# Performance work log

Hardware: AMD Instinct MI355X
Metric: run time of the kernel (lower is better)

The kernel has to match this reference:

```python
import jax, jax.numpy as jnp
import numpy as np

B, T, C, H, D = 128, 256, 384, 6, 64  # batch, seq (block_size), embed_dim, heads, head_size
FF = 4 * C


def _layernorm(x, g, b, eps=1e-5):
    mu = jnp.mean(x, axis=-1, keepdims=True)
    var = jnp.var(x, axis=-1, keepdims=True)
    return (x - mu) * jax.lax.rsqrt(var + eps) * g + b


def setup_inputs() -> dict:
    key = jax.random.key(0)
    ks = jax.random.split(key, 16)
    w = lambda k, shape: (jax.random.normal(k, shape, jnp.float32) * 0.02)
    return {
        "x": jax.random.normal(ks[0], (B, T, C), jnp.float32),
        "ln1_g": jnp.ones((C,), jnp.float32),
        "ln1_b": jnp.zeros((C,), jnp.float32),
        "Wk": w(ks[1], (H, C, D)), "bk": jnp.zeros((H, D), jnp.float32),
        "Wq": w(ks[2], (H, C, D)), "bq": jnp.zeros((H, D), jnp.float32),
        "Wv": w(ks[3], (H, C, D)), "bv": jnp.zeros((H, D), jnp.float32),
        "Wp": w(ks[4], (C, C)), "bp": jnp.zeros((C,), jnp.float32),
        "ln2_g": jnp.ones((C,), jnp.float32),
        "ln2_b": jnp.zeros((C,), jnp.float32),
        "W1": w(ks[5], (C, FF)), "b1": jnp.zeros((FF,), jnp.float32),
        "W2": w(ks[6], (FF, C)), "b2": jnp.zeros((C,), jnp.float32),
    }


def reference(x, ln1_g, ln1_b, Wk, bk, Wq, bq, Wv, bv, Wp, bp, ln2_g, ln2_b, W1, b1, W2, b2):
    # pre-LN attention branch
    h = _layernorm(x, ln1_g, ln1_b)
    # per-head projections, batched over heads: (B,T,C) x (H,C,D) -> (B,H,T,D)
    K = jnp.einsum("btc,hcd->bhtd", h, Wk) + bk[None, :, None, :]
    Q = jnp.einsum("btc,hcd->bhtd", h, Wq) + bq[None, :, None, :]
    V = jnp.einsum("btc,hcd->bhtd", h, Wv) + bv[None, :, None, :]
    # NOTE: original computes K @ Q^T scaled by embed_dim**-0.5 (faithful quirk)
    scores = jnp.einsum("bhtd,bhsd->bhts", K, Q) * (C ** -0.5)
    causal = jnp.tril(jnp.ones((T, T), dtype=bool))  # keep s <= t
    scores = jnp.where(causal[None, None], scores, -jnp.inf)
    attn = jax.nn.softmax(scores, axis=-1)  # dropout = identity (eval mode)
    out = jnp.einsum("bhts,bhsd->bhtd", attn, V)
    out = out.transpose(0, 2, 1, 3).reshape(B, T, C)  # concat heads
    x = x + out @ Wp + bp
    # pre-LN FFN branch
    h2 = _layernorm(x, ln2_g, ln2_b)
    x = x + jax.nn.relu(h2 @ W1 + b1) @ W2 + b2
    return x
```

## Files before the change

### kernel.cpp

```cpp
#include <hip/hip_runtime.h>
#include <stdint.h>

#define BB 128
#define TT 256
#define CC 384
#define HH 6
#define DD 64
#define FFF 1536
#define ROWS (BB*TT)

#define FCH 16384
#define NFC (ROWS/FCH)

typedef unsigned short u16;
typedef __bf16 bf8v __attribute__((ext_vector_type(8)));
typedef float f4v __attribute__((ext_vector_type(4)));

__device__ __forceinline__ float bf2f(u16 u) {
    unsigned int v = ((unsigned int)u) << 16;
    float f;
    __builtin_memcpy(&f, &v, 4);
    return f;
}
__device__ __forceinline__ u16 f2bf(float f) {
    unsigned int u;
    __builtin_memcpy(&u, &f, 4);
    u += 0x7fffu + ((u >> 16) & 1u);
    return (u16)(u >> 16);
}

__device__ __forceinline__ void gload_lds16(const void* g, void* l) {
    __builtin_amdgcn_global_load_lds(
        (__attribute__((address_space(1))) void*)(g),
        (__attribute__((address_space(3))) void*)(l), 16, 0, 0);
}

__device__ __forceinline__ void ln_body(
    int row, const float* __restrict__ x, const float* __restrict__ g,
    const float* __restrict__ b, u16* __restrict__ out, int lane)
{
    const float* xr = x + (long long)row * CC;
    float v[6]; float s = 0.f;
#pragma unroll
    for (int i = 0; i < 6; ++i) { v[i] = xr[lane + i * 64]; s += v[i]; }
#pragma unroll
    for (int o = 32; o > 0; o >>= 1) s += __shfl_xor(s, o);
    const float mu = s * (1.f / CC);
    float q = 0.f;
#pragma unroll
    for (int i = 0; i < 6; ++i) { float d = v[i] - mu; q += d * d; }
#pragma unroll
    for (int o = 32; o > 0; o >>= 1) q += __shfl_xor(q, o);
    const float inv = rsqrtf(q * (1.f / CC) + 1e-5f);
    u16* orow = out + (long long)row * CC;
#pragma unroll
    for (int i = 0; i < 6; ++i) {
        int c = lane + i * 64;
        orow[c] = f2bf((v[i] - mu) * inv * g[c] + b[c]);
    }
}

__global__ __launch_bounds__(256) void ln_kernel(
    const float* __restrict__ x, const float* __restrict__ g,
    const float* __restrict__ b, u16* __restrict__ out)
{
    ln_body(blockIdx.x * 4 + (threadIdx.x >> 6), x, g, b, out, threadIdx.x & 63);
}

__global__ __launch_bounds__(256) void ln1_cvt_kernel(
    const float* __restrict__ x, const float* __restrict__ ln1g, const float* __restrict__ ln1b,
    u16* __restrict__ h,
    const float* __restrict__ Wq, const float* __restrict__ Wk, const float* __restrict__ Wv,
    const float* __restrict__ bq, const float* __restrict__ bk, const float* __restrict__ bv,
    const float* __restrict__ Wp, const float* __restrict__ W1, const float* __restrict__ W2,
    u16* __restrict__ wqkvT, u16* __restrict__ wpT, u16* __restrict__ w1T,
    u16* __restrict__ w2T, float* __restrict__ bqkv)
{
    if (blockIdx.x < ROWS / 4) {
        ln_body(blockIdx.x * 4 + (threadIdx.x >> 6), x, ln1g, ln1b, h, threadIdx.x & 63);
        return;
    }
    const int S0 = 1152 * 384, S1 = 384 * 384, S2 = 1536 * 384, S3 = 384 * 1536;
    int i = (blockIdx.x - ROWS / 4) * 256 + threadIdx.x;
    if (i < S0) {
        int n = i / 384, k = i % 384;
        const float* W = (n < 384) ? Wq : (n < 768) ? Wk : Wv;
        int nn = (n >= 768) ? n - 768 : (n >= 384) ? n - 384 : n;
        int hh = nn >> 6, d = nn & 63;
        wqkvT[i] = f2bf(W[hh * (384 * 64) + k * 64 + d]);
        return;
    }
    i -= S0;
    if (i < S1) { int n = i / 384, k = i % 384; wpT[i] = f2bf(Wp[k * 384 + n]); return; }
    i -= S1;
    if (i < S2) { int n = i / 384, k = i % 384; w1T[i] = f2bf(W1[k * 1536 + n]); return; }
    i -= S2;
    if (i < S3) { int n = i / 1536, k = i % 1536; w2T[i] = f2bf(W2[k * 384 + n]); return; }
    i -= S3;
    if (i < 1152) bqkv[i] = (i < 384) ? bq[i] : (i < 768) ? bk[i - 384] : bv[i - 768];
}

__global__ __launch_bounds__(256) void vtrans_kernel(
    const u16* __restrict__ qkv, u16* __restrict__ vt)
{
    __shared__ u16 tile[64][65];
    const int z = blockIdx.x;
    const int tb = blockIdx.y;
    const int zb = z / HH, zh = z % HH;
    const u16* src = qkv + ((long long)(zb * TT + tb * 64)) * 1152 + 768 + zh * 64;
    const int tid = threadIdx.x;
#pragma unroll
    for (int it = 0; it < 16; ++it) {
        int idx = it * 256 + tid; int tl = idx >> 6, d = idx & 63;
        tile[tl][d] = src[(long long)tl * 1152 + d];
    }
    __syncthreads();
    u16* dst = vt + (long long)z * 64 * 256 + tb * 64;
#pragma unroll
    for (int it = 0; it < 16; ++it) {
        int idx = it * 256 + tid; int d = idx >> 6, tl = idx & 63;
        dst[(long long)d * 256 + tl] = tile[tl][d];
    }
}

__global__ __launch_bounds__(256) void flash_kernel(
    const u16* __restrict__ qkv, const u16* __restrict__ vt, u16* __restrict__ attnout)
{
    __shared__ __align__(16) u16 Pl[128 * 72];

    const int bh = blockIdx.x;
    const int half = blockIdx.y;
    const int b = bh / HH, hh = bh % HH;
    const int tid = threadIdx.x;
    const int wave = tid >> 6, lane = tid & 63;
    const int quad = lane >> 4, lq = lane & 15;
    const int t0 = half * 128;

    const long long qrow = (long long)b * TT * 1152;
    const u16* Kb  = qkv + qrow + 384 + hh * 64;
    const u16* Qb  = qkv + qrow + hh * 64;
    const u16* Vtb = vt + (long long)bh * (DD * TT);

    bf8v af[2][2];
#pragma unroll
    for (int i = 0; i < 2; ++i)
#pragma unroll
        for (int ks = 0; ks < 2; ++ks)
            af[i][ks] = *(const bf8v*)(Kb + (long long)(t0 + wave * 32 + i * 16 + lq) * 1152
                                          + ks * 32 + quad * 8);

    float m_run[2][4], l_run[2][4];
    f4v oacc[2][4];
#pragma unroll
    for (int i = 0; i < 2; ++i) {
#pragma unroll
        for (int r = 0; r < 4; ++r) { m_run[i][r] = -1e30f; l_run[i][r] = 0.f; }
#pragma unroll
        for (int j = 0; j < 4; ++j) oacc[i][j] = (f4v){0.f, 0.f, 0.f, 0.f};
    }

    const float scs = 0.05103103630798287f;
    const int ntiles = 2 * (half + 1);
    for (int st = 0; st < ntiles; ++st) {
        const int s0 = st * 64;
        f4v sacc[2][4];
#pragma unroll
        for (int i = 0; i < 2; ++i)
#pragma unroll
            for (int j = 0; j < 4; ++j) sacc[i][j] = (f4v){0.f, 0.f, 0.f, 0.f};
#pragma unroll
        for (int ks = 0; ks < 2; ++ks) {
            bf8v bq[4];
#pragma unroll
            for (int j = 0; j < 4; ++j)
                bq[j] = *(const bf8v*)(Qb + (long long)(s0 + j * 16 + lq) * 1152
                                          + ks * 32 + quad * 8);
#pragma unroll
            for (int i = 0; i < 2; ++i)
#pragma unroll
                for (int j = 0; j < 4; ++j)
                    sacc[i][j] = __builtin_amdgcn_mfma_f32_16x16x32_bf16(af[i][ks], bq[j], sacc[i][j], 0, 0, 0);
        }
#pragma unroll
        for (int i = 0; i < 2; ++i)
#pragma unroll
            for (int j = 0; j < 4; ++j)
#pragma unroll
                for (int r = 0; r < 4; ++r) {
                    int t_g = t0 + wave * 32 + i * 16 + quad * 4 + r;
                    int s_g = s0 + j * 16 + lq;
                    float v = sacc[i][j][r] * scs;
                    sacc[i][j][r] = (s_g <= t_g) ? v : -1e30f;
                }
#pragma unroll
        for (int i = 0; i < 2; ++i)
#pragma unroll
            for (int r = 0; r < 4; ++r) {
                float mt = sacc[i][0][r];
#pragma unroll
                for (int j = 1; j < 4; ++j) mt = fmaxf(mt, sacc[i][j][r]);
#pragma unroll
                for (int o = 8; o > 0; o >>= 1) mt = fmaxf(mt, __shfl_xor(mt, o));
                const float mn = fmaxf(m_run[i][r], mt);
                const float alpha = __expf(m_run[i][r] - mn);
                float rs = 0.f;
#pragma unroll
                for (int j = 0; j < 4; ++j) {
                    float e = __expf(sacc[i][j][r] - mn);
                    sacc[i][j][r] = e; rs += e;
                }
#pragma unroll
                for (int o = 8; o > 0; o >>= 1) rs += __shfl_xor(rs, o);
                m_run[i][r] = mn;
                l_run[i][r] = l_run[i][r] * alpha + rs;
#pragma unroll
                for (int j = 0; j < 4; ++j) oacc[i][j][r] *= alpha;
            }
#pragma unroll
        for (int i = 0; i < 2; ++i)
#pragma unroll
            for (int j = 0; j < 4; ++j)
#pragma unroll
                for (int r = 0; r < 4; ++r)
                    Pl[(wave * 32 + i * 16 + quad * 4 + r) * 72 + j * 16 + lq] = f2bf(sacc[i][j][r]);
#pragma unroll
        for (int ks2 = 0; ks2 < 2; ++ks2) {
            bf8v ap[2], bv_[4];
#pragma unroll
            for (int i = 0; i < 2; ++i)
                ap[i] = *(const bf8v*)(Pl + (wave * 32 + i * 16 + lq) * 72 + ks2 * 32 + quad * 8);
#pragma unroll
            for (int j = 0; j < 4; ++j)
                bv_[j] = *(const bf8v*)(Vtb + (long long)(j * 16 + lq) * 256 + s0 + ks2 * 32 + quad * 8);
#pragma unroll
            for (int i = 0; i < 2; ++i)
#pragma unroll
                for (int j = 0; j < 4; ++j)
                    oacc[i][j] = __builtin_amdgcn_mfma_f32_16x16x32_bf16(ap[i], bv_[j], oacc[i][j], 0, 0, 0);
        }
    }
#pragma unroll
    for (int i = 0; i < 2; ++i)
#pragma unroll
        for (int r = 0; r < 4; ++r) {
            const float inv = 1.f / l_run[i][r];
            u16* orow = attnout + ((long long)(b * TT + t0 + wave * 32 + i * 16 + quad * 4 + r)) * CC + hh * 64;
#pragma unroll
            for (int j = 0; j < 4; ++j)
                orow[j * 16 + lq] = f2bf(oacc[i][j][r] * inv);
        }
}

template<int BM, int BN, bool OUTBF, bool RELU, bool HASRES>
__global__ __launch_bounds__(256) void gemm_bt(
    const u16* __restrict__ A, const u16* __restrict__ Bw, void* __restrict__ Cp,
    const float* __restrict__ bias, const float* __restrict__ res,
    int K, int lda, int ldb, int ldc,
    long long sAb, long long sAh, long long sBb, long long sBh,
    long long sCb, long long sCh, int Hb, float scale)
{
    __shared__ __align__(16) u16 As[BM * 32];
    __shared__ __align__(16) u16 Bs[BN * 32];

    const int tid = threadIdx.x;
    const int wave = tid >> 6, lane = tid & 63;
    const int quad = lane >> 4, lq = lane & 15;

    const int z = blockIdx.z;
    const int zb = z / Hb, zh = z % Hb;
    const int m0 = blockIdx.x * BM;
    const int n0 = blockIdx.y * BN;

    A  += (long long)zb * sAb + (long long)zh * sAh + (long long)m0 * lda;
    Bw += (long long)zb * sBb + (long long)zh * sBh + (long long)n0 * ldb;
    const long long coff = (long long)zb * sCb + (long long)zh * sCh;

    constexpr int WM = BM / 2, WN = BN / 2;
    constexpr int MT = WM / 16, NT = WN / 16;
    const int wm0 = (wave >> 1) * WM;
    const int wn0 = (wave & 1) * WN;

    f4v acc[MT][NT];
#pragma unroll
    for (int i = 0; i < MT; ++i)
#pragma unroll
        for (int j = 0; j < NT; ++j) acc[i][j] = (f4v){0.f, 0.f, 0.f, 0.f};

    constexpr int AIT = BM / 64;
    constexpr int BIT = BN / 64;

    for (int k0 = 0; k0 < K; k0 += 32) {
        __syncthreads();
#pragma unroll
        for (int j = 0; j < AIT; ++j) {
            int idx = j * 256 + tid; int r = idx >> 2, pg = idx & 3;
            int lg = pg ^ ((r >> 1) & 3);
            gload_lds16(A + (long long)r * lda + k0 + lg * 8, As + idx * 8);
        }
#pragma unroll
        for (int j = 0; j < BIT; ++j) {
            int idx = j * 256 + tid; int r = idx >> 2, pg = idx & 3;
            int lg = pg ^ ((r >> 1) & 3);
            gload_lds16(Bw + (long long)r * ldb + k0 + lg * 8, Bs + idx * 8);
        }
        __syncthreads();

        bf8v af[MT], bfr[NT];
#pragma unroll
        for (int i = 0; i < MT; ++i) {
            int row = wm0 + i * 16 + lq;
            int pg = quad ^ ((row >> 1) & 3);
            af[i] = *(const bf8v*)(As + row * 32 + pg * 8);
        }
#pragma unroll
        for (int j = 0; j < NT; ++j) {
            int row = wn0 + j * 16 + lq;
            int pg = quad ^ ((row >> 1) & 3);
            bfr[j] = *(const bf8v*)(Bs + row * 32 + pg * 8);
        }
#pragma unroll
        for (int i = 0; i < MT; ++i)
#pragma unroll
            for (int j = 0; j < NT; ++j)
                acc[i][j] = __builtin_amdgcn_mfma_f32_16x16x32_bf16(af[i], bfr[j], acc[i][j], 0, 0, 0);
    }

#pragma unroll
    for (int i = 0; i < MT; ++i) {
#pragma unroll
        for (int j = 0; j < NT; ++j) {
            const int gcol = n0 + wn0 + j * 16 + lq;
            const float bcol = bias ? bias[gcol] : 0.f;
#pragma unroll
            for (int r = 0; r < 4; ++r) {
                const int grow = m0 + wm0 + i * 16 + quad * 4 + r;
                const long long off = coff + (long long)grow * ldc + gcol;
                float v = acc[i][j][r] * scale + bcol;
                if (HASRES) v += res[off];
                if (RELU)   v = fmaxf(v, 0.f);
                if (OUTBF)  ((u16*)Cp)[off] = f2bf(v);
                else        ((float*)Cp)[off] = v;
            }
        }
    }
}

extern "C" void kernel_launch(void* const* d_in, const int* in_sizes, int n_in,
                              void* d_out, int out_size, void* d_ws, size_t ws_size,
                              hipStream_t stream)
{
    const float* x    = (const float*)d_in[0];
    const float* ln1g = (const float*)d_in[1];
    const float* ln1b = (const float*)d_in[2];
    const float* Wk   = (const float*)d_in[3];
    const float* bk   = (const float*)d_in[4];
    const float* Wq   = (const float*)d_in[5];
    const float* bq   = (const float*)d_in[6];
    const float* Wv   = (const float*)d_in[7];
    const float* bv   = (const float*)d_in[8];
    const float* Wp   = (const float*)d_in[9];
    const float* bp   = (const float*)d_in[10];
    const float* ln2g = (const float*)d_in[11];
    const float* ln2b = (const float*)d_in[12];
    const float* W1   = (const float*)d_in[13];
    const float* b1   = (const float*)d_in[14];
    const float* W2   = (const float*)d_in[15];
    const float* b2   = (const float*)d_in[16];

    char* ws = (char*)d_ws;
    size_t off = 0;
    auto alloc = [&](size_t bytes) -> char* {
        char* p = ws + off; off += (bytes + 255) & ~(size_t)255; return p;
    };
    u16*   wqkvT = (u16*)alloc((size_t)1152 * 384 * 2);
    u16*   wpT   = (u16*)alloc((size_t)384 * 384 * 2);
    u16*   w1T   = (u16*)alloc((size_t)1536 * 384 * 2);
    u16*   w2T   = (u16*)alloc((size_t)384 * 1536 * 2);
    float* bqkv  = (float*)alloc((size_t)1152 * 4);
    u16*   h     = (u16*)alloc((size_t)ROWS * CC * 2);
    u16*   qkv   = (u16*)alloc((size_t)ROWS * 1152 * 2);
    u16*   vtff  = (u16*)alloc((size_t)FCH * FFF * 2);
    u16* attnout = h;
    u16* h2      = h;
    float* x1    = (float*)qkv;
    u16*   vt    = vtff;
    u16*   ff    = vtff;

    ln1_cvt_kernel<<<ROWS / 4 + 6918, 256, 0, stream>>>(
        x, ln1g, ln1b, h, Wq, Wk, Wv, bq, bk, bv, Wp, W1, W2,
        wqkvT, wpT, w1T, w2T, bqkv);
    gemm_bt<128, 128, true, false, false><<<dim3(ROWS / 128, 1152 / 128, 1), 256, 0, stream>>>(
        h, wqkvT, qkv, bqkv, nullptr, 384, 384, 384, 1152,
        0, 0, 0, 0, 0, 0, 1, 1.f);
    vtrans_kernel<<<dim3(BB * HH, 4), 256, 0, stream>>>(qkv, vt);
    flash_kernel<<<dim3(BB * HH, 2), 256, 0, stream>>>(qkv, vt, attnout);
    gemm_bt<128, 128, false, false, true><<<dim3(ROWS / 128, CC / 128, 1), 256, 0, stream>>>(
        attnout, wpT, x1, bp, x, CC, CC, CC, CC,
        0, 0, 0, 0, 0, 0, 1, 1.f);
    ln_kernel<<<ROWS / 4, 256, 0, stream>>>(x1, ln2g, ln2b, h2);
    for (int fc = 0; fc < NFC; ++fc) {
        const long long ro = (long long)fc * FCH;
        gemm_bt<128, 128, true, true, false><<<dim3(FCH / 128, FFF / 128, 1), 256, 0, stream>>>(
            h2 + ro * CC, w1T, ff, b1, nullptr, CC, CC, CC, FFF,
            0, 0, 0, 0, 0, 0, 1, 1.f);
        gemm_bt<128, 128, false, false, true><<<dim3(FCH / 128, CC / 128, 1), 256, 0, stream>>>(
            ff, w2T, (float*)d_out + ro * CC, b2, x1 + ro * CC, FFF, FFF, FFF, CC,
            0, 0, 0, 0, 0, 0, 1, 1.f);
    }
}
```

Before: 447.9 us.

## Split flash attention into 64-row query blocks and run FFN unchunked when workspace allows

The flash kernel now gives each block 64 query rows (16 per wave) instead of 128, launching four blocks per batch-head. The aim is better causal load balance and more, smaller blocks with fewer registers each. The FFN loop now runs as a single chunk when the workspace can hold the full intermediate, which removes one pair of GEMM launches and the partial-wave tails. The trade-off is less reuse of each K/V tile per block, so Q and V are loaded from global memory more times in total.

```diff
diff --git a/kernel.cpp b/kernel.cpp
--- a/kernel.cpp
+++ b/kernel.cpp
@@ -8,9 +8,6 @@
 #define DD 64
 #define FFF 1536
 #define ROWS (BB*TT)
-
-#define FCH 16384
-#define NFC (ROWS/FCH)
 
 typedef unsigned short u16;
 typedef __bf16 bf8v __attribute__((ext_vector_type(8)));
@@ -126,48 +123,41 @@
 __global__ __launch_bounds__(256) void flash_kernel(
     const u16* __restrict__ qkv, const u16* __restrict__ vt, u16* __restrict__ attnout)
 {
-    __shared__ __align__(16) u16 Pl[128 * 72];
-
-    const int bh = blockIdx.x;
-    const int half = blockIdx.y;
+    __shared__ __align__(16) u16 Pl[64 * 72];
+
+    const int blk = blockIdx.x;
+    const int bh = blk >> 2, q = blk & 3;
     const int b = bh / HH, hh = bh % HH;
     const int tid = threadIdx.x;
     const int wave = tid >> 6, lane = tid & 63;
     const int quad = lane >> 4, lq = lane & 15;
-    const int t0 = half * 128;
+    const int t0 = q * 64;
 
     const long long qrow = (long long)b * TT * 1152;
     const u16* Kb  = qkv + qrow + 384 + hh * 64;
     const u16* Qb  = qkv + qrow + hh * 64;
     const u16* Vtb = vt + (long long)bh * (DD * TT);
 
-    bf8v af[2][2];
-#pragma unroll
-    for (int i = 0; i < 2; ++i)
-#pragma unroll
-        for (int ks = 0; ks < 2; ++ks)
-            af[i][ks] = *(const bf8v*)(Kb + (long long)(t0 + wave * 32 + i * 16 + lq) * 1152
-                                          + ks * 32 + quad * 8);
-
-    float m_run[2][4], l_run[2][4];
-    f4v oacc[2][4];
-#pragma unroll
-    for (int i = 0; i < 2; ++i) {
-#pragma unroll
-        for (int r = 0; r < 4; ++r) { m_run[i][r] = -1e30f; l_run[i][r] = 0.f; }
-#pragma unroll
-        for (int j = 0; j < 4; ++j) oacc[i][j] = (f4v){0.f, 0.f, 0.f, 0.f};
-    }
+    bf8v af[2];
+#pragma unroll
+    for (int ks = 0; ks < 2; ++ks)
+        af[ks] = *(const bf8v*)(Kb + (long long)(t0 + wave * 16 + lq) * 1152
+                                    + ks * 32 + quad * 8);
+
+    float m_run[4], l_run[4];
+    f4v oacc[4];
+#pragma unroll
+    for (int r = 0; r < 4; ++r) { m_run[r] = -1e30f; l_run[r] = 0.f; }
+#pragma unroll
+    for (int j = 0; j < 4; ++j) oacc[j] = (f4v){0.f, 0.f, 0.f, 0.f};
 
     const float scs = 0.05103103630798287f;
-    const int ntiles = 2 * (half + 1);
+    const int ntiles = q + 1;
     for (int st = 0; st < ntiles; ++st) {
         const int s0 = st * 64;
-        f4v sacc[2][4];
-#pragma unroll
-        for (int i = 0; i < 2; ++i)
-#pragma unroll
-            for (int j = 0; j < 4; ++j) sacc[i][j] = (f4v){0.f, 0.f, 0.f, 0.f};
+        f4v sacc[4];
+#pragma unroll
+        for (int j = 0; j < 4; ++j) sacc[j] = (f4v){0.f, 0.f, 0.f, 0.f};
 #pragma unroll
         for (int ks = 0; ks < 2; ++ks) {
             bf8v bq[4];
@@ -176,79 +166,65 @@
                 bq[j] = *(const bf8v*)(Qb + (long long)(s0 + j * 16 + lq) * 1152
                                           + ks * 32 + quad * 8);
 #pragma unroll
-            for (int i = 0; i < 2; ++i)
-#pragma unroll
-                for (int j = 0; j < 4; ++j)
-                    sacc[i][j] = __builtin_amdgcn_mfma_f32_16x16x32_bf16(af[i][ks], bq[j], sacc[i][j], 0, 0, 0);
-        }
-#pragma unroll
-        for (int i = 0; i < 2; ++i)
-#pragma unroll
             for (int j = 0; j < 4; ++j)
-#pragma unroll
-                for (int r = 0; r < 4; ++r) {
-                    int t_g = t0 + wave * 32 + i * 16 + quad * 4 + r;
-                    int s_g = s0 + j * 16 + lq;
-                    float v = sacc[i][j][r] * scs;
-                    sacc[i][j][r] = (s_g <= t_g) ? v : -1e30f;
-                }
-#pragma unroll
-        for (int i = 0; i < 2; ++i)
+                sacc[j] = __builtin_amdgcn_mfma_f32_16x16x32_bf16(af[ks], bq[j], sacc[j], 0, 0, 0);
+        }
+#pragma unroll
+        for (int j = 0; j < 4; ++j)
 #pragma unroll
             for (int r = 0; r < 4; ++r) {
-                float mt = sacc[i][0][r];
-#pragma unroll
-                for (int j = 1; j < 4; ++j) mt = fmaxf(mt, sacc[i][j][r]);
-#pragma unroll
-                for (int o = 8; o > 0; o >>= 1) mt = fmaxf(mt, __shfl_xor(mt, o));
-                const float mn = fmaxf(m_run[i][r], mt);
-                const float alpha = __expf(m_run[i][r] - mn);
-                float rs = 0.f;
-#pragma unroll
-                for (int j = 0; j < 4; ++j) {
-                    float e = __expf(sacc[i][j][r] - mn);
-                    sacc[i][j][r] = e; rs += e;
-                }
-#pragma unroll
-                for (int o = 8; o > 0; o >>= 1) rs += __shfl_xor(rs, o);
-                m_run[i][r] = mn;
-                l_run[i][r] = l_run[i][r] * alpha + rs;
-#pragma unroll
-                for (int j = 0; j < 4; ++j) oacc[i][j][r] *= alpha;
+                int t_g = t0 + wave * 16 + quad * 4 + r;
+                int s_g = s0 + j * 16 + lq;
+                float v = sacc[j][r] * scs;
+                sacc[j][r] = (s_g <= t_g) ? v : -1e30f;
             }
 #pragma unroll
-        for (int i = 0; i < 2; ++i)
-#pragma unroll
-            for (int j = 0; j < 4; ++j)
-#pragma unroll
-                for (int r = 0; r < 4; ++r)
-                    Pl[(wave * 32 + i * 16 + quad * 4 + r) * 72 + j * 16 + lq] = f2bf(sacc[i][j][r]);
+        for (int r = 0; r < 4; ++r) {
+            float mt = sacc[0][r];
+#pragma unroll
+            for (int j = 1; j < 4; ++j) mt = fmaxf(mt, sacc[j][r]);
+#pragma unroll
+            for (int o = 8; o > 0; o >>= 1) mt = fmaxf(mt, __shfl_xor(mt, o));
+            const float mn = fmaxf(m_run[r], mt);
+            const float alpha = __expf(m_run[r] - mn);
+            float rs = 0.f;
+#pragma unroll
+            for (int j = 0; j < 4; ++j) {
+                float e = __expf(sacc[j][r] - mn);
+                sacc[j][r] = e; rs += e;
+            }
+#pragma unroll
+            for (int o = 8; o > 0; o >>= 1) rs += __shfl_xor(rs, o);
+            m_run[r] = mn;
+            l_run[r] = l_run[r] * alpha + rs;
+#pragma unroll
+            for (int j = 0; j < 4; ++j) oacc[j][r] *= alpha;
+        }
+#pragma unroll
+        for (int j = 0; j < 4; ++j)
+#pragma unroll
+            for (int r = 0; r < 4; ++r)
+                Pl[(wave * 16 + quad * 4 + r) * 72 + j * 16 + lq] = f2bf(sacc[j][r]);
 #pragma unroll
         for (int ks2 = 0; ks2 < 2; ++ks2) {
-            bf8v ap[2], bv_[4];
-#pragma unroll
-            for (int i = 0; i < 2; ++i)
-                ap[i] = *(const bf8v*)(Pl + (wave * 32 + i * 16 + lq) * 72 + ks2 * 32 + quad * 8);
+            bf8v ap = *(const bf8v*)(Pl + (wave * 16 + lq) * 72 + ks2 * 32 + quad * 8);
+            bf8v bv_[4];
 #pragma unroll
             for (int j = 0; j < 4; ++j)
                 bv_[j] = *(const bf8v*)(Vtb + (long long)(j * 16 + lq) * 256 + s0 + ks2 * 32 + quad * 8);
 #pragma unroll
-            for (int i = 0; i < 2; ++i)
-#pragma unroll
-                for (int j = 0; j < 4; ++j)
-                    oacc[i][j] = __builtin_amdgcn_mfma_f32_16x16x32_bf16(ap[i], bv_[j], oacc[i][j], 0, 0, 0);
-        }
-    }
-#pragma unroll
-    for (int i = 0; i < 2; ++i)
-#pragma unroll
-        for (int r = 0; r < 4; ++r) {
-            const float inv = 1.f / l_run[i][r];
-            u16* orow = attnout + ((long long)(b * TT + t0 + wave * 32 + i * 16 + quad * 4 + r)) * CC + hh * 64;
-#pragma unroll
             for (int j = 0; j < 4; ++j)
-                orow[j * 16 + lq] = f2bf(oacc[i][j][r] * inv);
-        }
+                oacc[j] = __builtin_amdgcn_mfma_f32_16x16x32_bf16(ap, bv_[j], oacc[j], 0, 0, 0);
+        }
+    }
+#pragma unroll
+    for (int r = 0; r < 4; ++r) {
+        const float inv = 1.f / l_run[r];
+        u16* orow = attnout + ((long long)(b * TT + t0 + wave * 16 + quad * 4 + r)) * CC + hh * 64;
+#pragma unroll
+        for (int j = 0; j < 4; ++j)
+            orow[j * 16 + lq] = f2bf(oacc[j][r] * inv);
+    }
 }
 
 template<int BM, int BN, bool OUTBF, bool RELU, bool HASRES>
@@ -379,12 +355,14 @@
     float* bqkv  = (float*)alloc((size_t)1152 * 4);
     u16*   h     = (u16*)alloc((size_t)ROWS * CC * 2);
     u16*   qkv   = (u16*)alloc((size_t)ROWS * 1152 * 2);
-    u16*   vtff  = (u16*)alloc((size_t)FCH * FFF * 2);
     u16* attnout = h;
     u16* h2      = h;
     float* x1    = (float*)qkv;
-    u16*   vt    = vtff;
-    u16*   ff    = vtff;
+    u16*   vt    = (u16*)(ws + off);
+    u16*   ff    = vt;
+    const size_t need_full = off + (size_t)ROWS * FFF * 2;
+    const int nfc = (ws_size >= need_full) ? 1 : 2;
+    const int fch = ROWS / nfc;
 
     ln1_cvt_kernel<<<ROWS / 4 + 6918, 256, 0, stream>>>(
         x, ln1g, ln1b, h, Wq, Wk, Wv, bq, bk, bv, Wp, W1, W2,
@@ -393,17 +371,17 @@
         h, wqkvT, qkv, bqkv, nullptr, 384, 384, 384, 1152,
         0, 0, 0, 0, 0, 0, 1, 1.f);
     vtrans_kernel<<<dim3(BB * HH, 4), 256, 0, stream>>>(qkv, vt);
-    flash_kernel<<<dim3(BB * HH, 2), 256, 0, stream>>>(qkv, vt, attnout);
+    flash_kernel<<<BB * HH * 4, 256, 0, stream>>>(qkv, vt, attnout);
     gemm_bt<128, 128, false, false, true><<<dim3(ROWS / 128, CC / 128, 1), 256, 0, stream>>>(
         attnout, wpT, x1, bp, x, CC, CC, CC, CC,
         0, 0, 0, 0, 0, 0, 1, 1.f);
     ln_kernel<<<ROWS / 4, 256, 0, stream>>>(x1, ln2g, ln2b, h2);
-    for (int fc = 0; fc < NFC; ++fc) {
-        const long long ro = (long long)fc * FCH;
-        gemm_bt<128, 128, true, true, false><<<dim3(FCH / 128, FFF / 128, 1), 256, 0, stream>>>(
+    for (int fc = 0; fc < nfc; ++fc) {
+        const long long ro = (long long)fc * fch;
+        gemm_bt<128, 128, true, true, false><<<dim3(fch / 128, FFF / 128, 1), 256, 0, stream>>>(
             h2 + ro * CC, w1T, ff, b1, nullptr, CC, CC, CC, FFF,
             0, 0, 0, 0, 0, 0, 1, 1.f);
-        gemm_bt<128, 128, false, false, true><<<dim3(FCH / 128, CC / 128, 1), 256, 0, stream>>>(
+        gemm_bt<128, 128, false, false, true><<<dim3(fch / 128, CC / 128, 1), 256, 0, stream>>>(
             ff, w2T, (float*)d_out + ro * CC, b2, x1 + ro * CC, FFF, FFF, FFF, CC,
             0, 0, 0, 0, 0, 0, 1, 1.f);
     }
```

After: 475.6 us. 1.06x slower.

## Stage Q/V tiles in swizzled LDS in flash kernel; adapt FFN chunking to workspace

Applied to the files above, without the earlier changes.

The flash kernel now cooperatively loads each 64x64 Q tile and V^T tile into shared memory with async global-to-LDS copies and an XOR swizzle, and reads MFMA operands from LDS instead of issuing redundant strided global loads per wave. The grid is flattened so the two halves of each (batch, head) are adjacent blocks, which may help L2 reuse. The FFN chunk count is chosen at runtime from the workspace size, so the whole FFN runs in one pass when space allows. The kernel gains two barriers per tile and no double buffering, so load latency is not hidden.

```diff
diff --git a/kernel.cpp b/kernel.cpp
--- a/kernel.cpp
+++ b/kernel.cpp
@@ -8,9 +8,6 @@
 #define DD 64
 #define FFF 1536
 #define ROWS (BB*TT)
-
-#define FCH 16384
-#define NFC (ROWS/FCH)
 
 typedef unsigned short u16;
 typedef __bf16 bf8v __attribute__((ext_vector_type(8)));
@@ -126,10 +123,12 @@
 __global__ __launch_bounds__(256) void flash_kernel(
     const u16* __restrict__ qkv, const u16* __restrict__ vt, u16* __restrict__ attnout)
 {
+    __shared__ __align__(16) u16 Qs[64 * 64];
+    __shared__ __align__(16) u16 Vs[64 * 64];
     __shared__ __align__(16) u16 Pl[128 * 72];
 
-    const int bh = blockIdx.x;
-    const int half = blockIdx.y;
+    const int blk = blockIdx.x;
+    const int bh = blk >> 1, half = blk & 1;
     const int b = bh / HH, hh = bh % HH;
     const int tid = threadIdx.x;
     const int wave = tid >> 6, lane = tid & 63;
@@ -163,6 +162,21 @@
     const int ntiles = 2 * (half + 1);
     for (int st = 0; st < ntiles; ++st) {
         const int s0 = st * 64;
+        __syncthreads();
+#pragma unroll
+        for (int it = 0; it < 2; ++it) {
+            int idx = it * 256 + tid; int r = idx >> 3, pg = idx & 7;
+            int lg = pg ^ (r & 7);
+            gload_lds16(Qb + (long long)(s0 + r) * 1152 + lg * 8, Qs + idx * 8);
+        }
+#pragma unroll
+        for (int it = 0; it < 2; ++it) {
+            int idx = it * 256 + tid; int r = idx >> 3, pg = idx & 7;
+            int lg = pg ^ (r & 7);
+            gload_lds16(Vtb + (long long)r * 256 + s0 + lg * 8, Vs + idx * 8);
+        }
+        __syncthreads();
+
         f4v sacc[2][4];
 #pragma unroll
         for (int i = 0; i < 2; ++i)
@@ -172,9 +186,11 @@
         for (int ks = 0; ks < 2; ++ks) {
             bf8v bq[4];
 #pragma unroll
-            for (int j = 0; j < 4; ++j)
-                bq[j] = *(const bf8v*)(Qb + (long long)(s0 + j * 16 + lq) * 1152
-                                          + ks * 32 + quad * 8);
+            for (int j = 0; j < 4; ++j) {
+                int row = j * 16 + lq;
+                int p = (ks * 4 + quad) ^ (row & 7);
+                bq[j] = *(const bf8v*)(Qs + row * 64 + p * 8);
+            }
 #pragma unroll
             for (int i = 0; i < 2; ++i)
 #pragma unroll
@@ -230,8 +246,11 @@
             for (int i = 0; i < 2; ++i)
                 ap[i] = *(const bf8v*)(Pl + (wave * 32 + i * 16 + lq) * 72 + ks2 * 32 + quad * 8);
 #pragma unroll
-            for (int j = 0; j < 4; ++j)
-                bv_[j] = *(const bf8v*)(Vtb + (long long)(j * 16 + lq) * 256 + s0 + ks2 * 32 + quad * 8);
+            for (int j = 0; j < 4; ++j) {
+                int row = j * 16 + lq;
+                int p = (ks2 * 4 + quad) ^ (row & 7);
+                bv_[j] = *(const bf8v*)(Vs + row * 64 + p * 8);
+            }
 #pragma unroll
             for (int i = 0; i < 2; ++i)
 #pragma unroll
@@ -379,12 +398,14 @@
     float* bqkv  = (float*)alloc((size_t)1152 * 4);
     u16*   h     = (u16*)alloc((size_t)ROWS * CC * 2);
     u16*   qkv   = (u16*)alloc((size_t)ROWS * 1152 * 2);
-    u16*   vtff  = (u16*)alloc((size_t)FCH * FFF * 2);
     u16* attnout = h;
     u16* h2      = h;
     float* x1    = (float*)qkv;
-    u16*   vt    = vtff;
-    u16*   ff    = vtff;
+    u16*   vt    = (u16*)(ws + off);
+    u16*   ff    = vt;
+    const size_t need_full = off + (size_t)ROWS * FFF * 2;
+    const int nfc = (ws_size >= need_full) ? 1 : 2;
+    const int fch = ROWS / nfc;
 
     ln1_cvt_kernel<<<ROWS / 4 + 6918, 256, 0, stream>>>(
         x, ln1g, ln1b, h, Wq, Wk, Wv, bq, bk, bv, Wp, W1, W2,
@@ -393,17 +414,17 @@
         h, wqkvT, qkv, bqkv, nullptr, 384, 384, 384, 1152,
         0, 0, 0, 0, 0, 0, 1, 1.f);
     vtrans_kernel<<<dim3(BB * HH, 4), 256, 0, stream>>>(qkv, vt);
-    flash_kernel<<<dim3(BB * HH, 2), 256, 0, stream>>>(qkv, vt, attnout);
+    flash_kernel<<<BB * HH * 2, 256, 0, stream>>>(qkv, vt, attnout);
     gemm_bt<128, 128, false, false, true><<<dim3(ROWS / 128, CC / 128, 1), 256, 0, stream>>>(
         attnout, wpT, x1, bp, x, CC, CC, CC, CC,
         0, 0, 0, 0, 0, 0, 1, 1.f);
     ln_kernel<<<ROWS / 4, 256, 0, stream>>>(x1, ln2g, ln2b, h2);
-    for (int fc = 0; fc < NFC; ++fc) {
-        const long long ro = (long long)fc * FCH;
-        gemm_bt<128, 128, true, true, false><<<dim3(FCH / 128, FFF / 128, 1), 256, 0, stream>>>(
+    for (int fc = 0; fc < nfc; ++fc) {
+        const long long ro = (long long)fc * fch;
+        gemm_bt<128, 128, true, true, false><<<dim3(fch / 128, FFF / 128, 1), 256, 0, stream>>>(
             h2 + ro * CC, w1T, ff, b1, nullptr, CC, CC, CC, FFF,
             0, 0, 0, 0, 0, 0, 1, 1.f);
-        gemm_bt<128, 128, false, false, true><<<dim3(FCH / 128, CC / 128, 1), 256, 0, stream>>>(
+        gemm_bt<128, 128, false, false, true><<<dim3(fch / 128, CC / 128, 1), 256, 0, stream>>>(
             ff, w2T, (float*)d_out + ro * CC, b2, x1 + ro * CC, FFF, FFF, FFF, CC,
             0, 0, 0, 0, 0, 0, 1, 1.f);
     }
```

Result: faster. 436.8 us (-2.5%).
